# Optimization experiments

Hardware: AMD Instinct MI355X
Metric: run time of the kernel (lower is better)

The kernel has to match this reference:

```python
import jax, jax.numpy as jnp
import numpy as np

B, N, D = 4, 4096, 768
SCALE = 1.0 / np.sqrt(D).astype(np.float32)


def setup_inputs() -> dict:
    key = jax.random.key(0)
    k1, k2, k3 = jax.random.split(key, 3)
    x = jax.random.normal(k1, (B, N, D), dtype=jnp.float32)
    w_qkv = jax.random.normal(k2, (D, 3 * D), dtype=jnp.float32) * (1.0 / np.sqrt(D))
    b_qkv = jnp.zeros((3 * D,), dtype=jnp.float32)
    w_out = jax.random.normal(k3, (D, D), dtype=jnp.float32) * (1.0 / np.sqrt(D))
    b_out = jnp.zeros((D,), dtype=jnp.float32)
    return {"x": x, "w_qkv": w_qkv, "b_qkv": b_qkv, "w_out": w_out, "b_out": b_out}


def reference(x, w_qkv, b_qkv, w_out, b_out):
    # fused QKV projection: [B,N,3D]
    qkv = jnp.einsum("bnd,de->bne", x, w_qkv) + b_qkv
    q, k, v = jnp.split(qkv, 3, axis=-1)          # each [B,N,D]
    # scaled dot-product attention (single head)
    scores = jnp.einsum("bnd,bmd->bnm", q, k) * SCALE  # [B,N,N]
    attn = jax.nn.softmax(scores, axis=-1)
    ctx = jnp.einsum("bnm,bmd->bnd", attn, v)          # [B,N,D]
    out = jnp.einsum("bnd,de->bne", ctx, w_out) + b_out
    return out
```

## Files before the change

### kernel.cpp

```cpp
#include <hip/hip_runtime.h>
#include <cstdint>
#include <cstddef>

#define BB 4
#define NN 4096
#define DD 768
#define EE 2304
#define MTOT 16384
static constexpr float ATT_SCALE = 0.03608439182435161f;

typedef _Float16 v8h __attribute__((ext_vector_type(8)));
typedef _Float16 v4h __attribute__((ext_vector_type(4)));
typedef float v4f __attribute__((ext_vector_type(4)));

__device__ __forceinline__ void async_copy16(void* lds, const void* gmem) {
  __builtin_amdgcn_global_load_lds(
      (const __attribute__((address_space(1))) uint32_t*)(uintptr_t)gmem,
      (__attribute__((address_space(3))) uint32_t*)(uintptr_t)lds,
      16, 0, 0);
}

enum { EPI_QKV = 0, EPI_F16 = 1, EPI_OUT = 2, EPI_PV = 3 };

template <int EPI>
__global__ __launch_bounds__(256) void gemm128(
    const _Float16* __restrict__ A, int lda, size_t zA,
    const _Float16* __restrict__ Bt, int ldb, size_t zB,
    int K,
    float* __restrict__ c_f32,
    _Float16* __restrict__ c_f16,
    int ldc, size_t zC, size_t chalf,
    const float* __restrict__ bias,
    _Float16* __restrict__ q_out,
    _Float16* __restrict__ k_out,
    _Float16* __restrict__ v_out) {
  __shared__ __align__(16) _Float16 As[128 * 64];
  __shared__ __align__(16) _Float16 Bs[128 * 64];

  const int tid = threadIdx.x;
  const int wid = tid >> 6, lane = tid & 63;
  const int wr = wid >> 1, wc = wid & 1;
  const int lq = lane >> 4, lr = lane & 15;
  const int m0 = blockIdx.x * 128, n0 = blockIdx.y * 128;
  const int z = blockIdx.z;
  int bidx, koff;
  if constexpr (EPI == EPI_PV) {
    bidx = z & 1;
    koff = (z >> 1) * K;
  } else {
    bidx = z;
    koff = 0;
  }

  const _Float16* Ab = A + (size_t)bidx * zA + (size_t)m0 * lda + koff;
  const _Float16* Bb = Bt + (size_t)bidx * zB + (size_t)n0 * ldb + koff;

  v4f acc[4][4] = {};

  for (int k0 = 0; k0 < K; k0 += 64) {
#pragma unroll
    for (int i = 0; i < 4; ++i) {
      const int c = i * 256 + tid;
      const int r = c >> 3;
      const int kc = (c & 7) ^ (r & 7);
      async_copy16(As + (size_t)c * 8, Ab + (size_t)r * lda + (k0 + kc * 8));
      async_copy16(Bs + (size_t)c * 8, Bb + (size_t)r * ldb + (k0 + kc * 8));
    }
    __syncthreads();

#pragma unroll
    for (int ks = 0; ks < 2; ++ks) {
      v8h af[4], bf[4];
#pragma unroll
      for (int t = 0; t < 4; ++t) {
        const int ra = wr * 64 + t * 16 + lr;
        const int rb = wc * 64 + t * 16 + lr;
        const int cb = ks * 4 + lq;
        af[t] = *(const v8h*)(As + ra * 64 + (((cb ^ (ra & 7)) << 3)));
        bf[t] = *(const v8h*)(Bs + rb * 64 + (((cb ^ (rb & 7)) << 3)));
      }
#pragma unroll
      for (int mt = 0; mt < 4; ++mt)
#pragma unroll
        for (int nt = 0; nt < 4; ++nt)
          acc[mt][nt] = __builtin_amdgcn_mfma_f32_16x16x32_f16(
              af[mt], bf[nt], acc[mt][nt], 0, 0, 0);
    }
    __syncthreads();
  }

  float* cf = nullptr;
  _Float16* ch = nullptr;
  if constexpr (EPI == EPI_PV)
    cf = c_f32 + (size_t)(z >> 1) * chalf + (size_t)bidx * zC;
  else if constexpr (EPI == EPI_OUT)
    cf = c_f32 + (size_t)bidx * zC;
  else if constexpr (EPI == EPI_F16)
    ch = c_f16 + (size_t)bidx * zC;

#pragma unroll
  for (int mt = 0; mt < 4; ++mt) {
#pragma unroll
    for (int nt = 0; nt < 4; ++nt) {
#pragma unroll
      for (int rg = 0; rg < 4; ++rg) {
        const int gm = m0 + wr * 64 + mt * 16 + lq * 4 + rg;
        const int gn = n0 + wc * 64 + nt * 16 + lr;
        float v = acc[mt][nt][rg];
        if constexpr (EPI == EPI_QKV) {
          v += bias[gn];
          if (gn < DD) {
            q_out[(size_t)gm * DD + gn] = (_Float16)(v * ATT_SCALE);
          } else if (gn < 2 * DD) {
            k_out[(size_t)gm * DD + (gn - DD)] = (_Float16)v;
          } else {
            v_out[(size_t)gm * DD + (gn - 2 * DD)] = (_Float16)v;
          }
        } else if constexpr (EPI == EPI_F16) {
          ch[(size_t)gm * ldc + gn] = (_Float16)v;
        } else {
          cf[(size_t)gm * ldc + gn] = (EPI == EPI_OUT) ? v + bias[gn] : v;
        }
      }
    }
  }
}

__global__ __launch_bounds__(256) void reduce_ctx(const float* __restrict__ h0,
                                                  const float* __restrict__ h1,
                                                  _Float16* __restrict__ out,
                                                  int n4) {
  int i = blockIdx.x * blockDim.x + threadIdx.x;
  if (i < n4) {
    v4f a = ((const v4f*)h0)[i];
    v4f b = ((const v4f*)h1)[i];
    v4h o;
#pragma unroll
    for (int j = 0; j < 4; ++j) o[j] = (_Float16)(a[j] + b[j]);
    ((v4h*)out)[i] = o;
  }
}

__global__ __launch_bounds__(256) void softmax_rows_f16(_Float16* __restrict__ S) {
  _Float16* row = S + (size_t)blockIdx.y * NN * NN + (size_t)blockIdx.x * NN;
  const int tid = threadIdx.x;
  const int lane = tid & 63, wid = tid >> 6;

  float f[16];
  float m = -3.0e38f;
#pragma unroll
  for (int i = 0; i < 2; ++i) {
    v8h v = ((const v8h*)row)[tid + i * 256];
#pragma unroll
    for (int j = 0; j < 8; ++j) {
      f[i * 8 + j] = (float)v[j];
      m = fmaxf(m, f[i * 8 + j]);
    }
  }
#pragma unroll
  for (int off = 32; off > 0; off >>= 1) m = fmaxf(m, __shfl_xor(m, off));
  __shared__ float redm[4], reds[4];
  if (lane == 0) redm[wid] = m;
  __syncthreads();
  m = fmaxf(fmaxf(redm[0], redm[1]), fmaxf(redm[2], redm[3]));

  float sum = 0.f;
#pragma unroll
  for (int i = 0; i < 16; ++i) {
    f[i] = __expf(f[i] - m);
    sum += f[i];
  }
#pragma unroll
  for (int off = 32; off > 0; off >>= 1) sum += __shfl_xor(sum, off);
  if (lane == 0) reds[wid] = sum;
  __syncthreads();
  sum = reds[0] + reds[1] + reds[2] + reds[3];
  const float inv = 1.0f / sum;
#pragma unroll
  for (int i = 0; i < 2; ++i) {
    v8h o;
#pragma unroll
    for (int j = 0; j < 8; ++j) o[j] = (_Float16)(f[i * 8 + j] * inv);
    ((v8h*)row)[tid + i * 256] = o;
  }
}

__global__ __launch_bounds__(256) void cvt_f16(const float* __restrict__ in,
                                               _Float16* __restrict__ out, int n4) {
  int i = blockIdx.x * blockDim.x + threadIdx.x;
  if (i < n4) {
    v4f v = ((const v4f*)in)[i];
    v4h o;
#pragma unroll
    for (int j = 0; j < 4; ++j) o[j] = (_Float16)v[j];
    ((v4h*)out)[i] = o;
  }
}

__global__ __launch_bounds__(256) void transpose_cvt(const float* __restrict__ in,
                                                     _Float16* __restrict__ out,
                                                     int R, int C) {
  __shared__ float tile[32][33];
  const int bx = blockIdx.x * 32;
  const int by = blockIdx.y * 32;
  const int tx = threadIdx.x & 31, ty = threadIdx.x >> 5;
#pragma unroll
  for (int i = 0; i < 32; i += 8)
    tile[ty + i][tx] = in[(size_t)(by + ty + i) * C + (bx + tx)];
  __syncthreads();
#pragma unroll
  for (int i = 0; i < 32; i += 8)
    out[(size_t)(bx + ty + i) * R + (by + tx)] = (_Float16)tile[tx][ty + i];
}

__global__ __launch_bounds__(256) void transpose_v(const _Float16* __restrict__ in,
                                                   _Float16* __restrict__ out) {
  __shared__ _Float16 tile[32][33];
  const int b = blockIdx.z;
  const _Float16* src = in + (size_t)b * NN * DD;
  _Float16* dst = out + (size_t)b * NN * DD;
  const int bx = blockIdx.x * 32;
  const int by = blockIdx.y * 32;
  const int tx = threadIdx.x & 31, ty = threadIdx.x >> 5;
#pragma unroll
  for (int i = 0; i < 32; i += 8)
    tile[ty + i][tx] = src[(size_t)(by + ty + i) * DD + (bx + tx)];
  __syncthreads();
#pragma unroll
  for (int i = 0; i < 32; i += 8)
    dst[(size_t)(bx + ty + i) * NN + (by + tx)] = tile[tx][ty + i];
}

extern "C" void kernel_launch(void* const* d_in, const int* in_sizes, int n_in,
                              void* d_out, int out_size, void* d_ws, size_t ws_size,
                              hipStream_t stream) {
  const float* x = (const float*)d_in[0];
  const float* w_qkv = (const float*)d_in[1];
  const float* b_qkv = (const float*)d_in[2];
  const float* w_out = (const float*)d_in[3];
  const float* b_out = (const float*)d_in[4];
  float* out = (float*)d_out;
  char* ws = (char*)d_ws;

  _Float16* xh    = (_Float16*)(ws + 0);
  _Float16* wqkvh = (_Float16*)(ws + 25165824);
  _Float16* wouth = (_Float16*)(ws + 28704768);
  _Float16* Qh    = (_Float16*)(ws + 29884416);
  _Float16* Kh    = (_Float16*)(ws + 55050240);
  _Float16* Vh    = (_Float16*)(ws + 80216064);
  _Float16* Sh    = (_Float16*)(ws + 105381888);
  _Float16* Vth   = (_Float16*)(ws + 0);
  _Float16* Ch    = (_Float16*)(ws + 80216064);

  const size_t zQK = (size_t)NN * DD;
  const size_t zS = (size_t)NN * NN;
  const size_t zCtx = (size_t)NN * DD;
  const size_t chalf = 2 * zCtx;

  cvt_f16<<<dim3((MTOT * DD / 4) / 256), 256, 0, stream>>>(x, xh, MTOT * DD / 4);
  transpose_cvt<<<dim3(EE / 32, DD / 32), 256, 0, stream>>>(w_qkv, wqkvh, DD, EE);
  transpose_cvt<<<dim3(DD / 32, DD / 32), 256, 0, stream>>>(w_out, wouth, DD, DD);

  gemm128<EPI_QKV><<<dim3(MTOT / 128, EE / 128), 256, 0, stream>>>(
      xh, DD, 0, wqkvh, DD, 0, DD, nullptr, nullptr, 0, 0, 0, b_qkv, Qh, Kh, Vh);

  transpose_v<<<dim3(DD / 32, NN / 32, BB), 256, 0, stream>>>(Vh, Vth);

  for (int c = 0; c < BB / 2; ++c) {
    const _Float16* Qc = Qh + (size_t)c * 2 * zQK;
    const _Float16* Kc = Kh + (size_t)c * 2 * zQK;
    const _Float16* Vtc = Vth + (size_t)c * 2 * zQK;
    gemm128<EPI_F16><<<dim3(NN / 128, NN / 128, 2), 256, 0, stream>>>(
        Qc, DD, zQK, Kc, DD, zQK, DD, nullptr, Sh, NN, zS, 0, nullptr, nullptr,
        nullptr, nullptr);
    softmax_rows_f16<<<dim3(NN, 2), 256, 0, stream>>>(Sh);
    gemm128<EPI_PV><<<dim3(NN / 128, DD / 128, 4), 256, 0, stream>>>(
        Sh, NN, zS, Vtc, NN, zQK, NN / 2, out, nullptr, DD, zCtx, chalf,
        nullptr, nullptr, nullptr, nullptr);
    reduce_ctx<<<dim3((int)(chalf / 4 / 256)), 256, 0, stream>>>(
        out, out + chalf, Ch + (size_t)c * 2 * zQK, (int)(chalf / 4));
  }

  gemm128<EPI_OUT><<<dim3(MTOT / 128, DD / 128), 256, 0, stream>>>(
      Ch, DD, 0, wouth, DD, 0, DD, out, nullptr, DD, 0, 0, b_out, nullptr,
      nullptr, nullptr);
}
```

Measured before the change: 568.2 us.

## Replace 128x128 GEMM with 256x256 tile, 4-stage async LDS pipeline, 512 threads

The GEMM kernel now uses 256x256 output tiles with 8 waves and a K step of 32. Global-to-LDS loads run through a 4-slot ring buffer with explicit vmcnt waits, so loads for future K steps overlap MFMA work and each step needs one barrier. It also raises MFMA priority during compute and uses a new XOR swizzle for 32-wide rows. The larger tiles cut global traffic per flop, but each wave holds 128 accumulator registers and grids get smaller (e.g. PV gets 16x3x4 blocks), which may hurt occupancy and load balance on small problems.

```diff
diff --git a/kernel.cpp b/kernel.cpp
--- a/kernel.cpp
+++ b/kernel.cpp
@@ -20,10 +20,12 @@
       16, 0, 0);
 }
 
+#define WAIT_VMCNT(n) asm volatile("s_waitcnt vmcnt(" #n ")" ::: "memory")
+
 enum { EPI_QKV = 0, EPI_F16 = 1, EPI_OUT = 2, EPI_PV = 3 };
 
 template <int EPI>
-__global__ __launch_bounds__(256) void gemm128(
+__global__ __launch_bounds__(512, 2) void gemm256(
     const _Float16* __restrict__ A, int lda, size_t zA,
     const _Float16* __restrict__ Bt, int ldb, size_t zB,
     int K,
@@ -34,14 +36,14 @@
     _Float16* __restrict__ q_out,
     _Float16* __restrict__ k_out,
     _Float16* __restrict__ v_out) {
-  __shared__ __align__(16) _Float16 As[128 * 64];
-  __shared__ __align__(16) _Float16 Bs[128 * 64];
+  __shared__ __align__(16) _Float16 As[4][256 * 32];
+  __shared__ __align__(16) _Float16 Bs[4][256 * 32];
 
   const int tid = threadIdx.x;
   const int wid = tid >> 6, lane = tid & 63;
-  const int wr = wid >> 1, wc = wid & 1;
+  const int wr = wid >> 2, wc = wid & 3;
   const int lq = lane >> 4, lr = lane & 15;
-  const int m0 = blockIdx.x * 128, n0 = blockIdx.y * 128;
+  const int m0 = blockIdx.x * 256, n0 = blockIdx.y * 256;
   const int z = blockIdx.z;
   int bidx, koff;
   if constexpr (EPI == EPI_PV) {
@@ -55,38 +57,69 @@
   const _Float16* Ab = A + (size_t)bidx * zA + (size_t)m0 * lda + koff;
   const _Float16* Bb = Bt + (size_t)bidx * zB + (size_t)n0 * ldb + koff;
 
-  v4f acc[4][4] = {};
-
-  for (int k0 = 0; k0 < K; k0 += 64) {
-#pragma unroll
-    for (int i = 0; i < 4; ++i) {
-      const int c = i * 256 + tid;
-      const int r = c >> 3;
-      const int kc = (c & 7) ^ (r & 7);
-      async_copy16(As + (size_t)c * 8, Ab + (size_t)r * lda + (k0 + kc * 8));
-      async_copy16(Bs + (size_t)c * 8, Bb + (size_t)r * ldb + (k0 + kc * 8));
+  const int c0 = tid, c1 = tid + 512;
+  const int r0 = c0 >> 2, r1 = c1 >> 2;
+  const int k0c = ((c0 & 3) ^ ((r0 >> 1) & 3)) << 3;
+  const int k1c = ((c1 & 3) ^ ((r1 >> 1) & 3)) << 3;
+  const size_t ga0 = (size_t)r0 * lda + k0c, ga1 = (size_t)r1 * lda + k1c;
+  const size_t gb0 = (size_t)r0 * ldb + k0c, gb1 = (size_t)r1 * ldb + k1c;
+
+  int aoff[8], boff[4];
+#pragma unroll
+  for (int t = 0; t < 8; ++t) {
+    const int ra = wr * 128 + t * 16 + lr;
+    aoff[t] = ra * 32 + ((lq ^ ((ra >> 1) & 3)) << 3);
+  }
+#pragma unroll
+  for (int n = 0; n < 4; ++n) {
+    const int rb = wc * 64 + n * 16 + lr;
+    boff[n] = rb * 32 + ((lq ^ ((rb >> 1) & 3)) << 3);
+  }
+
+  v4f acc[8][4] = {};
+  const int NT = K / 32;
+
+  auto stage = [&](int slot, int kt) {
+    const int kk = kt * 32;
+    async_copy16(&As[slot][c0 * 8], Ab + ga0 + kk);
+    async_copy16(&As[slot][c1 * 8], Ab + ga1 + kk);
+    async_copy16(&Bs[slot][c0 * 8], Bb + gb0 + kk);
+    async_copy16(&Bs[slot][c1 * 8], Bb + gb1 + kk);
+  };
+
+  stage(0, 0);
+  stage(1, 1);
+  stage(2, 2);
+
+  for (int it = 0; it < NT; ++it) {
+    if (it < NT - 2) {
+      WAIT_VMCNT(8);
+    } else if (it == NT - 2) {
+      WAIT_VMCNT(4);
+    } else {
+      WAIT_VMCNT(0);
     }
-    __syncthreads();
-
-#pragma unroll
-    for (int ks = 0; ks < 2; ++ks) {
-      v8h af[4], bf[4];
-#pragma unroll
-      for (int t = 0; t < 4; ++t) {
-        const int ra = wr * 64 + t * 16 + lr;
-        const int rb = wc * 64 + t * 16 + lr;
-        const int cb = ks * 4 + lq;
-        af[t] = *(const v8h*)(As + ra * 64 + (((cb ^ (ra & 7)) << 3)));
-        bf[t] = *(const v8h*)(Bs + rb * 64 + (((cb ^ (rb & 7)) << 3)));
-      }
-#pragma unroll
-      for (int mt = 0; mt < 4; ++mt)
-#pragma unroll
-        for (int nt = 0; nt < 4; ++nt)
-          acc[mt][nt] = __builtin_amdgcn_mfma_f32_16x16x32_f16(
-              af[mt], bf[nt], acc[mt][nt], 0, 0, 0);
-    }
-    __syncthreads();
+    __builtin_amdgcn_s_barrier();
+    __builtin_amdgcn_sched_barrier(0);
+
+    if (it + 3 < NT) stage((it + 3) & 3, it + 3);
+
+    const _Float16* Asl = As[it & 3];
+    const _Float16* Bsl = Bs[it & 3];
+    v8h af[8], bf[4];
+#pragma unroll
+    for (int t = 0; t < 8; ++t) af[t] = *(const v8h*)(Asl + aoff[t]);
+#pragma unroll
+    for (int n = 0; n < 4; ++n) bf[n] = *(const v8h*)(Bsl + boff[n]);
+
+    __builtin_amdgcn_s_setprio(1);
+#pragma unroll
+    for (int mt = 0; mt < 8; ++mt)
+#pragma unroll
+      for (int nt = 0; nt < 4; ++nt)
+        acc[mt][nt] = __builtin_amdgcn_mfma_f32_16x16x32_f16(
+            af[mt], bf[nt], acc[mt][nt], 0, 0, 0);
+    __builtin_amdgcn_s_setprio(0);
   }
 
   float* cf = nullptr;
@@ -99,12 +132,12 @@
     ch = c_f16 + (size_t)bidx * zC;
 
 #pragma unroll
-  for (int mt = 0; mt < 4; ++mt) {
+  for (int mt = 0; mt < 8; ++mt) {
 #pragma unroll
     for (int nt = 0; nt < 4; ++nt) {
 #pragma unroll
       for (int rg = 0; rg < 4; ++rg) {
-        const int gm = m0 + wr * 64 + mt * 16 + lq * 4 + rg;
+        const int gm = m0 + wr * 128 + mt * 16 + lq * 4 + rg;
         const int gn = n0 + wc * 64 + nt * 16 + lr;
         float v = acc[mt][nt][rg];
         if constexpr (EPI == EPI_QKV) {
@@ -261,7 +294,7 @@
   transpose_cvt<<<dim3(EE / 32, DD / 32), 256, 0, stream>>>(w_qkv, wqkvh, DD, EE);
   transpose_cvt<<<dim3(DD / 32, DD / 32), 256, 0, stream>>>(w_out, wouth, DD, DD);
 
-  gemm128<EPI_QKV><<<dim3(MTOT / 128, EE / 128), 256, 0, stream>>>(
+  gemm256<EPI_QKV><<<dim3(MTOT / 256, EE / 256), 512, 0, stream>>>(
       xh, DD, 0, wqkvh, DD, 0, DD, nullptr, nullptr, 0, 0, 0, b_qkv, Qh, Kh, Vh);
 
   transpose_v<<<dim3(DD / 32, NN / 32, BB), 256, 0, stream>>>(Vh, Vth);
@@ -270,18 +303,18 @@
     const _Float16* Qc = Qh + (size_t)c * 2 * zQK;
     const _Float16* Kc = Kh + (size_t)c * 2 * zQK;
     const _Float16* Vtc = Vth + (size_t)c * 2 * zQK;
-    gemm128<EPI_F16><<<dim3(NN / 128, NN / 128, 2), 256, 0, stream>>>(
+    gemm256<EPI_F16><<<dim3(NN / 256, NN / 256, 2), 512, 0, stream>>>(
         Qc, DD, zQK, Kc, DD, zQK, DD, nullptr, Sh, NN, zS, 0, nullptr, nullptr,
         nullptr, nullptr);
     softmax_rows_f16<<<dim3(NN, 2), 256, 0, stream>>>(Sh);
-    gemm128<EPI_PV><<<dim3(NN / 128, DD / 128, 4), 256, 0, stream>>>(
+    gemm256<EPI_PV><<<dim3(NN / 256, DD / 256, 4), 512, 0, stream>>>(
         Sh, NN, zS, Vtc, NN, zQK, NN / 2, out, nullptr, DD, zCtx, chalf,
         nullptr, nullptr, nullptr, nullptr);
     reduce_ctx<<<dim3((int)(chalf / 4 / 256)), 256, 0, stream>>>(
         out, out + chalf, Ch + (size_t)c * 2 * zQK, (int)(chalf / 4));
   }
 
-  gemm128<EPI_OUT><<<dim3(MTOT / 128, DD / 128), 256, 0, stream>>>(
+  gemm256<EPI_OUT><<<dim3(MTOT / 256, DD / 256), 512, 0, stream>>>(
       Ch, DD, 0, wouth, DD, 0, DD, out, nullptr, DD, 0, 0, b_out, nullptr,
       nullptr, nullptr);
 }
```

After: 557.4 us. About the same (-1.9%).
